# Kernel optimization log

Measured on AMD Instinct MI355X. Metric: run time of the kernel, lower is better.

## Reference

```python
import jax, jax.numpy as jnp
import numpy as np

H = 1024          # hidden_size
A = 8             # num_actions
T = 64            # timesteps
N = 256           # batch (num envs)


def _gru_cell(x, h, Wih, Whh, bih, bhh):
    # torch.nn.GRUCell math; gate order (r, z, n)
    gi = x @ Wih.T + bih           # [N, 3H]
    gh = h @ Whh.T + bhh           # [N, 3H]
    i_r, i_z, i_n = jnp.split(gi, 3, axis=1)
    h_r, h_z, h_n = jnp.split(gh, 3, axis=1)
    r = jax.nn.sigmoid(i_r + h_r)
    z = jax.nn.sigmoid(i_z + h_z)
    n = jnp.tanh(i_n + r * h_n)
    return (1.0 - z) * n + z * h


def setup_inputs() -> dict:
    key = jax.random.key(0)
    ks = jax.random.split(key, 12)
    s = 0.02
    return {
        "c": jax.random.normal(ks[0], (T * N, H), jnp.float32),
        "hxs": jax.random.normal(ks[1], (N, 3 * H), jnp.float32),
        "masks": jnp.ones((T * N, 1), jnp.float32),
        "prev_action_one_hot": jnp.zeros((T * N, A), jnp.float32).at[jnp.arange(T * N), jax.random.randint(ks[2], (T * N,), 0, A)].set(1.0),
        "h_gru_Wih": s * jax.random.normal(ks[3], (3 * H, H), jnp.float32),
        "h_gru_Whh": s * jax.random.normal(ks[4], (3 * H, H), jnp.float32),
        "h_gru_bih": jnp.zeros((3 * H,), jnp.float32),
        "h_gru_bhh": jnp.zeros((3 * H,), jnp.float32),
        "f_gru_Wih": s * jax.random.normal(ks[5], (3 * H, H), jnp.float32),
        "f_gru_Whh": s * jax.random.normal(ks[6], (3 * H, H), jnp.float32),
        "f_gru_bih": jnp.zeros((3 * H,), jnp.float32),
        "f_gru_bhh": jnp.zeros((3 * H,), jnp.float32),
        "p_W": s * jax.random.normal(ks[7], (2 * H, 2 * H + A), jnp.float32),
        "p_b": jnp.zeros((2 * H,), jnp.float32),
        "q_W": s * jax.random.normal(ks[8], (2 * H, 2 * H + A), jnp.float32),
        "q_b": jnp.zeros((2 * H,), jnp.float32),
    }


def reference(c, hxs, masks, prev_action_one_hot,
              h_gru_Wih, h_gru_Whh, h_gru_bih, h_gru_bhh,
              f_gru_Wih, f_gru_Whh, f_gru_bih, f_gru_bhh,
              p_W, p_b, q_W, q_b):
    c3 = c.reshape(T, N, H)
    m3 = masks.reshape(T, N, 1)
    a3 = prev_action_one_hot.reshape(T, N, A)
    f0 = hxs[:, :H]
    h0 = hxs[:, H:2 * H]
    q0 = hxs[:, 2 * H:]

    def step(carry, xs):
        f, h, q_mu = carry
        c_t, m_t, a_t = xs
        p_in = jnp.concatenate([h, q_mu, a_t], axis=1) * m_t
        p_dist = p_in @ p_W.T + p_b                     # [N, 2H]
        p_mu = p_dist[:, :H]
        q_in = jnp.concatenate([f, c_t, a_t], axis=1) * m_t
        q_dist = q_in @ q_W.T + q_b                     # [N, 2H]
        q_mu_new = q_dist[:, :H]
        f_new = _gru_cell(c_t, f * m_t, f_gru_Wih, f_gru_Whh, f_gru_bih, f_gru_bhh)
        h_new = _gru_cell(p_mu, h * m_t, h_gru_Wih, h_gru_Whh, h_gru_bih, h_gru_bhh)
        return (f_new, h_new, q_mu_new), (p_dist, q_dist)

    (f, h, q_mu), (p_all, q_all) = jax.lax.scan(step, (f0, h0, q0), (c3, m3, a3))
    acc_p = p_all.reshape(T * N, 2 * H)
    acc_q = q_all.reshape(T * N, 2 * H)
    hxs_out = jnp.concatenate([f, h, q_mu], axis=1)
    return acc_p, acc_q, hxs_out
```

## Files before the change

### kernel.cpp

```cpp
#include <hip/hip_runtime.h>
#include <math.h>

typedef __attribute__((ext_vector_type(8))) __bf16 bf16x8;
typedef __attribute__((ext_vector_type(4))) float f32x4;

constexpr int H = 1024, T = 64, NB = 256, TWOH = 2048, THREEH = 3072;
constexpr long long OFF_Q  = 33554432LL;
constexpr long long OFF_HX = 67108864LL;
constexpr int LA = 6;

constexpr int R_PWH = 0, R_PWQ = 2048, R_QWF = 4096, R_QWC = 6144,
              R_FWIH = 8192, R_FWHH = 11264, R_HWIH = 14336, R_HWHH = 17408;

#define LD4(p) (*reinterpret_cast<const float4*>(p))

__device__ __forceinline__ float sigf(float x) { return 1.0f / (1.0f + expf(-x)); }

__device__ __forceinline__ void gload16(const void* g, void* l) {
    __builtin_amdgcn_global_load_lds(
        (const __attribute__((address_space(1))) uint32_t*)g,
        (__attribute__((address_space(3))) uint32_t*)l, 16, 0, 0);
}

__device__ __forceinline__ void st_bf_swz(__bf16* base, int n, int k, float v) {
    base[(size_t)n * 1024 + (((k >> 3) ^ (n & 7)) << 3) + (k & 7)] = (__bf16)v;
}

#define FRAGOFF(rloc, gl) (((rloc) << 7) + ((((gl)) ^ ((rloc) & 7)) << 4))

template<int RT>
__device__ __forceinline__ void stage_tile(const char* g, char* l, int kb, int tid) {
    #pragma unroll
    for (int i = 0; i < RT / 32; ++i) {
        const int L = i * 4096 + tid * 16;
        gload16(g + (size_t)(L >> 7) * 2048 + (size_t)kb * 128 + (L & 127), l + L);
    }
}

__device__ __forceinline__ void mm128(
    int tid, char* sA, char* sB,
    const char* A, const char* B, int nit,
    f32x4 (&acc)[2][4])
{
    const int lane = tid & 63, w = tid >> 6;
    const int l15 = lane & 15, lg = lane >> 4;
    const int wr = w >> 1, wc = w & 1;
    int aoff[2][2], boff[4][2];
    #pragma unroll
    for (int fr = 0; fr < 2; ++fr)
        #pragma unroll
        for (int kk = 0; kk < 2; ++kk)
            aoff[fr][kk] = FRAGOFF(wr * 32 + fr * 16 + l15, kk * 4 + lg);
    #pragma unroll
    for (int fc = 0; fc < 4; ++fc)
        #pragma unroll
        for (int kk = 0; kk < 2; ++kk)
            boff[fc][kk] = FRAGOFF(wc * 64 + fc * 16 + l15, kk * 4 + lg);

    stage_tile<64>(A, sA, 0, tid);
    stage_tile<128>(B, sB, 0, tid);
    if (nit > 1) {
        stage_tile<64>(A, sA + 8192, 1, tid);
        stage_tile<128>(B, sB + 16384, 1, tid);
    }
    for (int kb = 0; kb < nit; ++kb) {
        const int kn = kb + 2;
        if (kn < nit) {
            const int bo = kn % 3;
            stage_tile<64>(A, sA + bo * 8192, kn, tid);
            stage_tile<128>(B, sB + bo * 16384, kn, tid);
            asm volatile("s_waitcnt vmcnt(12)" ::: "memory");
        } else if (kb + 1 < nit) {
            asm volatile("s_waitcnt vmcnt(6)" ::: "memory");
        } else {
            asm volatile("s_waitcnt vmcnt(0)" ::: "memory");
        }
        __builtin_amdgcn_s_barrier();
        __builtin_amdgcn_sched_barrier(0);
        const int bc = kb % 3;
        char* Ab = sA + bc * 8192;
        char* Bb = sB + bc * 16384;
        bf16x8 af[2][2], bv[4][2];
        #pragma unroll
        for (int fr = 0; fr < 2; ++fr)
            #pragma unroll
            for (int kk = 0; kk < 2; ++kk)
                af[fr][kk] = *reinterpret_cast<const bf16x8*>(Ab + aoff[fr][kk]);
        #pragma unroll
        for (int fc = 0; fc < 4; ++fc)
            #pragma unroll
            for (int kk = 0; kk < 2; ++kk)
                bv[fc][kk] = *reinterpret_cast<const bf16x8*>(Bb + boff[fc][kk]);
        __builtin_amdgcn_s_setprio(1);
        #pragma unroll
        for (int kk = 0; kk < 2; ++kk)
            #pragma unroll
            for (int fr = 0; fr < 2; ++fr)
                #pragma unroll
                for (int fc = 0; fc < 4; ++fc)
                    acc[fr][fc] = __builtin_amdgcn_mfma_f32_16x16x32_bf16(
                        af[fr][kk], bv[fc][kk], acc[fr][fc], 0, 0, 0);
        __builtin_amdgcn_s_setprio(0);
        __builtin_amdgcn_s_barrier();
        __builtin_amdgcn_sched_barrier(0);
    }
}

__device__ __forceinline__ void mm32g1(
    int tid, char* sA, char* sB,
    const char* A, const char* Bg,
    f32x4 (&aR)[2], f32x4 (&aZ)[2], f32x4 (&aN)[2])
{
    const int lane = tid & 63, w = tid >> 6;
    const int l15 = lane & 15, lg = lane >> 4;
    const int wr = w >> 1, wc = w & 1;
    int aoff[2], boff[2][2];
    #pragma unroll
    for (int kk = 0; kk < 2; ++kk)
        aoff[kk] = FRAGOFF(wr * 16 + l15, kk * 4 + lg);
    #pragma unroll
    for (int fc = 0; fc < 2; ++fc)
        #pragma unroll
        for (int kk = 0; kk < 2; ++kk)
            boff[fc][kk] = FRAGOFF(wc * 32 + fc * 16 + l15, kk * 4 + lg);

    auto stg = [&](int buf, int kb) {
        stage_tile<32>(A, sA + buf * 4096, kb, tid);
        #pragma unroll
        for (int g = 0; g < 3; ++g)
            stage_tile<64>(Bg + (size_t)g * 2097152, sB + buf * 24576 + g * 8192, kb, tid);
    };
    stg(0, 0);
    for (int kb = 0; kb < 16; ++kb) {
        if (kb + 1 < 16) {
            stg((kb + 1) & 1, kb + 1);
            asm volatile("s_waitcnt vmcnt(7)" ::: "memory");
        } else {
            asm volatile("s_waitcnt vmcnt(0)" ::: "memory");
        }
        __builtin_amdgcn_s_barrier();
        __builtin_amdgcn_sched_barrier(0);
        char* Ab = sA + (kb & 1) * 4096;
        char* Bb = sB + (kb & 1) * 24576;
        bf16x8 af[2];
        #pragma unroll
        for (int kk = 0; kk < 2; ++kk)
            af[kk] = *reinterpret_cast<const bf16x8*>(Ab + aoff[kk]);
        bf16x8 bvr[2][2], bvz[2][2], bvn[2][2];
        #pragma unroll
        for (int fc = 0; fc < 2; ++fc)
            #pragma unroll
            for (int kk = 0; kk < 2; ++kk) {
                bvr[fc][kk] = *reinterpret_cast<const bf16x8*>(Bb + boff[fc][kk]);
                bvz[fc][kk] = *reinterpret_cast<const bf16x8*>(Bb + 8192 + boff[fc][kk]);
                bvn[fc][kk] = *reinterpret_cast<const bf16x8*>(Bb + 16384 + boff[fc][kk]);
            }
        __builtin_amdgcn_s_setprio(1);
        #pragma unroll
        for (int kk = 0; kk < 2; ++kk)
            #pragma unroll
            for (int fc = 0; fc < 2; ++fc) {
                aR[fc] = __builtin_amdgcn_mfma_f32_16x16x32_bf16(af[kk], bvr[fc][kk], aR[fc], 0, 0, 0);
                aZ[fc] = __builtin_amdgcn_mfma_f32_16x16x32_bf16(af[kk], bvz[fc][kk], aZ[fc], 0, 0, 0);
                aN[fc] = __builtin_amdgcn_mfma_f32_16x16x32_bf16(af[kk], bvn[fc][kk], aN[fc], 0, 0, 0);
            }
        __builtin_amdgcn_s_setprio(0);
        __builtin_amdgcn_s_barrier();
        __builtin_amdgcn_sched_barrier(0);
    }
}

__device__ __forceinline__ void do_xq(int slice, int i, int tid, char* sA, char* sB,
    const char* cbfB, const char* Wb, const float* act, const float* qW, float* out)
{
    const int lane = tid & 63, w = tid >> 6;
    const int l15 = lane & 15, lg = lane >> 4;
    const int wr = w >> 1, wc = w & 1;
    const int row0 = (i >> 4) * 64, col0 = (i & 15) * 128;
    const size_t grow0 = (size_t)slice * NB + row0;
    f32x4 acc[2][4] = {};
    mm128(tid, sA, sB, cbfB + grow0 * 2048, Wb + (size_t)(R_QWC + col0) * 2048, 16, acc);
    #pragma unroll
    for (int fc = 0; fc < 4; ++fc) {
        const int gc = col0 + wc * 64 + fc * 16 + l15;
        const float* wp = qW + (size_t)gc * 2056 + 2048;
        float4 x0 = LD4(wp), x1 = LD4(wp + 4);
        #pragma unroll
        for (int fr = 0; fr < 2; ++fr)
            #pragma unroll
            for (int j = 0; j < 4; ++j) {
                const size_t n = grow0 + wr * 32 + fr * 16 + lg * 4 + j;
                const float* ar = act + n * 8;
                float4 a0 = LD4(ar), a1 = LD4(ar + 4);
                float dot = a0.x * x0.x + a0.y * x0.y + a0.z * x0.z + a0.w * x0.w
                          + a1.x * x1.x + a1.y * x1.y + a1.z * x1.z + a1.w * x1.w;
                out[OFF_Q + n * TWOH + gc] = acc[fr][fc][j] + dot;
            }
    }
}

__device__ __forceinline__ void do_gf(int slice, int i, int tid, char* sA, char* sB,
    const char* cbfB, const char* Wb, __bf16* Gfb)
{
    const int lane = tid & 63, w = tid >> 6;
    const int l15 = lane & 15, lg = lane >> 4;
    const int wr = w >> 1, wc = w & 1;
    const int row0 = (i / 24) * 64, col0 = (i % 24) * 128;
    f32x4 acc[2][4] = {};
    mm128(tid, sA, sB, cbfB + ((size_t)slice * NB + row0) * 2048,
          Wb + (size_t)(R_FWIH + col0) * 2048, 16, acc);
    __bf16* gdst = Gfb + (size_t)(slice & 7) * NB * THREEH;
    #pragma unroll
    for (int fc = 0; fc < 4; ++fc) {
        const int gc = col0 + wc * 64 + fc * 16 + l15;
        #pragma unroll
        for (int fr = 0; fr < 2; ++fr)
            #pragma unroll
            for (int j = 0; j < 4; ++j) {
                const int n = row0 + wr * 32 + fr * 16 + lg * 4 + j;
                gdst[(size_t)n * THREEH + gc] = (__bf16)acc[fr][fc][j];
            }
    }
}

__device__ __forceinline__ void do_pq(int tt, int i, int tid, char* sA, char* sB,
    const __bf16* qmu_t, const char* Wb, const float* masks, const float* act,
    const float* pW, const float* pb, float* out)
{
    const int lane = tid & 63, w = tid >> 6;
    const int l15 = lane & 15, lg = lane >> 4;
    const int wr = w >> 1, wc = w & 1;
    const int row0 = (i >> 4) * 64, col0 = (i & 15) * 128;
    f32x4 acc[2][4] = {};
    mm128(tid, sA, sB, (const char*)qmu_t + (size_t)row0 * 2048,
          Wb + (size_t)(R_PWQ + col0) * 2048, 16, acc);
    const float* mrow = masks + (size_t)tt * NB;
    float* ob = out + (size_t)tt * NB * TWOH;
    #pragma unroll
    for (int fc = 0; fc < 4; ++fc) {
        const int gc = col0 + wc * 64 + fc * 16 + l15;
        const float* wp = pW + (size_t)gc * 2056 + 2048;
        float4 x0 = LD4(wp), x1 = LD4(wp + 4);
        const float bb = pb[gc];
        #pragma unroll
        for (int fr = 0; fr < 2; ++fr)
            #pragma unroll
            for (int j = 0; j < 4; ++j) {
                const int n = row0 + wr * 32 + fr * 16 + lg * 4 + j;
                const float* ar = act + ((size_t)tt * NB + n) * 8;
                float4 a0 = LD4(ar), a1 = LD4(ar + 4);
                float dot = a0.x * x0.x + a0.y * x0.y + a0.z * x0.z + a0.w * x0.w
                          + a1.x * x1.x + a1.y * x1.y + a1.z * x1.z + a1.w * x1.w;
                ob[(size_t)n * TWOH + gc] = acc[fr][fc][j] + mrow[n] * dot + bb;
            }
    }
}

__global__ __launch_bounds__(256) void wcvt_k(
    const float* __restrict__ pW, const float* __restrict__ qW,
    const float* __restrict__ fWih, const float* __restrict__ fWhh,
    const float* __restrict__ hWih, const float* __restrict__ hWhh,
    __bf16* __restrict__ Wbf)
{
    const long i = (long)blockIdx.x * 256 + threadIdx.x;
    const int row = (int)(i >> 7);
    const int G   = (int)i & 127;
    const float* src; int stride; int koff = 0; int r;
    if (row < 2048)       { src = pW;   stride = 2056; koff = 0;    r = row; }
    else if (row < 4096)  { src = pW;   stride = 2056; koff = 1024; r = row - 2048; }
    else if (row < 6144)  { src = qW;   stride = 2056; koff = 0;    r = row - 4096; }
    else if (row < 8192)  { src = qW;   stride = 2056; koff = 1024; r = row - 6144; }
    else if (row < 11264) { src = fWih; stride = 1024; r = row - 8192; }
    else if (row < 14336) { src = fWhh; stride = 1024; r = row - 11264; }
    else if (row < 17408) { src = hWih; stride = 1024; r = row - 14336; }
    else                  { src = hWhh; stride = 1024; r = row - 17408; }
    const float* p = src + (long)r * stride + koff + G * 8;
    float4 a = LD4(p), b = LD4(p + 4);
    bf16x8 v;
    v[0] = (__bf16)a.x; v[1] = (__bf16)a.y; v[2] = (__bf16)a.z; v[3] = (__bf16)a.w;
    v[4] = (__bf16)b.x; v[5] = (__bf16)b.y; v[6] = (__bf16)b.z; v[7] = (__bf16)b.w;
    *reinterpret_cast<bf16x8*>(Wbf + (size_t)row * 1024 + ((G ^ (row & 7)) << 3)) = v;
}

__global__ __launch_bounds__(256) void ccvt_k(const float* __restrict__ c,
                                              __bf16* __restrict__ cbf) {
    const long i = (long)blockIdx.x * 256 + threadIdx.x;
    const int row = (int)(i >> 7);
    const int G   = (int)i & 127;
    const float* p = c + (size_t)row * 1024 + G * 8;
    float4 a = LD4(p), b = LD4(p + 4);
    bf16x8 v;
    v[0] = (__bf16)a.x; v[1] = (__bf16)a.y; v[2] = (__bf16)a.z; v[3] = (__bf16)a.w;
    v[4] = (__bf16)b.x; v[5] = (__bf16)b.y; v[6] = (__bf16)b.z; v[7] = (__bf16)b.w;
    *reinterpret_cast<bf16x8*>(cbf + (size_t)row * 1024 + ((G ^ (row & 7)) << 3)) = v;
}

__global__ __launch_bounds__(256) void init2_k(
    const float* __restrict__ hxs, const float* __restrict__ masks,
    float* __restrict__ fst0, float* __restrict__ hst0,
    __bf16* __restrict__ fbm0, __bf16* __restrict__ hbm0, __bf16* __restrict__ qmub0)
{
    const int idx = blockIdx.x * 256 + threadIdx.x;
    const int arr = idx >> 15;
    const int g   = idx & 32767;
    const int n   = g >> 7;
    const int G   = g & 127;
    const float m0 = masks[n];
    const float* p = hxs + (size_t)n * THREEH + arr * 1024 + G * 8;
    float4 a = LD4(p), b = LD4(p + 4);
    __bf16* dstB = arr == 0 ? fbm0 : (arr == 1 ? hbm0 : qmub0);
    bf16x8 v;
    v[0] = (__bf16)(a.x * m0); v[1] = (__bf16)(a.y * m0);
    v[2] = (__bf16)(a.z * m0); v[3] = (__bf16)(a.w * m0);
    v[4] = (__bf16)(b.x * m0); v[5] = (__bf16)(b.y * m0);
    v[6] = (__bf16)(b.z * m0); v[7] = (__bf16)(b.w * m0);
    *reinterpret_cast<bf16x8*>(dstB + (size_t)n * 1024 + ((G ^ (n & 7)) << 3)) = v;
    if (arr < 2) {
        float* dstF = arr == 0 ? fst0 : hst0;
        *reinterpret_cast<float4*>(dstF + (size_t)n * 1024 + G * 8) = a;
        *reinterpret_cast<float4*>(dstF + (size_t)n * 1024 + G * 8 + 4) = b;
    }
}

__global__ __launch_bounds__(256) void pre_k(
    const char* __restrict__ cbfB, const char* __restrict__ Wb,
    const float* __restrict__ act, const float* __restrict__ qW,
    const __bf16* __restrict__ qmb0, const float* __restrict__ masks,
    const float* __restrict__ pW, const float* __restrict__ pb,
    __bf16* __restrict__ Gfb, float* __restrict__ out)
{
    __shared__ char smem[73728];
    if (blockIdx.x < LA * 160) {
        const int s = blockIdx.x / 160;
        const int i = blockIdx.x % 160;
        if (i < 64) do_xq(s, i, threadIdx.x, smem, smem + 24576, cbfB, Wb, act, qW, out);
        else        do_gf(s, i - 64, threadIdx.x, smem, smem + 24576, cbfB, Wb, Gfb);
    } else {
        do_pq(0, blockIdx.x - LA * 160, threadIdx.x, smem, smem + 24576,
              qmb0, Wb, masks, act, pW, pb, out);
    }
}

__global__ __launch_bounds__(256) void k1_k(
    int t,
    const __bf16* __restrict__ hbm, const __bf16* __restrict__ fbm,
    __bf16* __restrict__ qmubN,
    const float* __restrict__ masks, const float* __restrict__ act,
    const float* __restrict__ qb, const float* __restrict__ qW,
    const char* __restrict__ Wb,
    __bf16* __restrict__ pmub, float* __restrict__ Shh,
    const __bf16* __restrict__ Gfb,
    const float* __restrict__ fbih, const float* __restrict__ fbhh,
    const float* __restrict__ fstF, float* __restrict__ fstN, __bf16* __restrict__ fbmN,
    float* __restrict__ out)
{
    __shared__ char smem[73728];
    char* sA = smem;
    char* sB = smem + 24576;
    const int tid = threadIdx.x;
    const int lane = tid & 63, w = tid >> 6;
    const int l15 = lane & 15, lg = lane >> 4;
    const int wr = w >> 1, wc = w & 1;
    const float* mrow = masks + (size_t)t * NB;
    const float* mn   = masks + (size_t)(t + 1 < T ? t + 1 : t) * NB;
    int b = blockIdx.x;

    if (b < 64) {
        const int row0 = (b >> 4) * 64, col0 = (b & 15) * 128;
        f32x4 acc[2][4] = {};
        mm128(tid, sA, sB,
              (const char*)hbm + (size_t)row0 * 2048,
              Wb + (size_t)(R_PWH + col0) * 2048, 16, acc);
        float* ob = out + (size_t)t * NB * TWOH;
        #pragma unroll
        for (int fc = 0; fc < 4; ++fc) {
            const int gc = col0 + wc * 64 + fc * 16 + l15;
            #pragma unroll
            for (int fr = 0; fr < 2; ++fr)
                #pragma unroll
                for (int j = 0; j < 4; ++j) {
                    const int n = row0 + wr * 32 + fr * 16 + lg * 4 + j;
                    const float v = ob[(size_t)n * TWOH + gc] + acc[fr][fc][j];
                    ob[(size_t)n * TWOH + gc] = v;
                    if (gc < 1024) st_bf_swz(pmub, n, gc, v);
                }
        }
    } else if (b < 128) {
        b -= 64;
        const int row0 = (b >> 4) * 64, col0 = (b & 15) * 128;
        f32x4 acc[2][4] = {};
        mm128(tid, sA, sB,
              (const char*)fbm + (size_t)row0 * 2048,
              Wb + (size_t)(R_QWF + col0) * 2048, 16, acc);
        float* ob = out + OFF_Q + (size_t)t * NB * TWOH;
        #pragma unroll
        for (int fc = 0; fc < 4; ++fc) {
            const int gc = col0 + wc * 64 + fc * 16 + l15;
            const float bb = qb[gc];
            #pragma unroll
            for (int fr = 0; fr < 2; ++fr)
                #pragma unroll
                for (int j = 0; j < 4; ++j) {
                    const int n = row0 + wr * 32 + fr * 16 + lg * 4 + j;
                    const float xq = ob[(size_t)n * TWOH + gc];
                    float v = acc[fr][fc][j] + mrow[n] * xq + bb;
                    ob[(size_t)n * TWOH + gc] = v;
                    if (gc < 1024) st_bf_swz(qmubN, n, gc, v * mn[n]);
                }
        }
    } else if (b < 224) {
        const int i = b - 128;
        const int row0 = (i / 24) * 64, col0 = (i % 24) * 128;
        f32x4 acc[2][4] = {};
        mm128(tid, sA, sB,
              (const char*)hbm + (size_t)row0 * 2048,
              Wb + (size_t)(R_HWHH + col0) * 2048, 16, acc);
        #pragma unroll
        for (int fc = 0; fc < 4; ++fc) {
            const int gc = col0 + wc * 64 + fc * 16 + l15;
            #pragma unroll
            for (int fr = 0; fr < 2; ++fr)
                #pragma unroll
                for (int j = 0; j < 4; ++j) {
                    const int n = row0 + wr * 32 + fr * 16 + lg * 4 + j;
                    Shh[(size_t)n * THREEH + gc] = acc[fr][fc][j];
                }
        }
    } else {
        const int i = b - 224;
        const int row0 = (i >> 4) * 32, col0 = (i & 15) * 64;
        f32x4 aR[2] = {}, aZ[2] = {}, aN[2] = {};
        mm32g1(tid, sA, sB,
               (const char*)fbm + (size_t)row0 * 2048,
               Wb + (size_t)(R_FWHH + col0) * 2048, aR, aZ, aN);
        const __bf16* gsl = Gfb + (size_t)(t & 7) * NB * THREEH;
        #pragma unroll
        for (int fc = 0; fc < 2; ++fc) {
            const int col = col0 + wc * 32 + fc * 16 + l15;
            const float br  = fbih[col] + fbhh[col];
            const float bz  = fbih[col + 1024] + fbhh[col + 1024];
            const float bni = fbih[col + 2048], bnh = fbhh[col + 2048];
            #pragma unroll
            for (int j = 0; j < 4; ++j) {
                const int n = row0 + wr * 16 + lg * 4 + j;
                const float gfr = (float)gsl[(size_t)n * THREEH + col];
                const float gfz = (float)gsl[(size_t)n * THREEH + col + 1024];
                const float gfn = (float)gsl[(size_t)n * THREEH + col + 2048];
                const float rg = sigf(gfr + aR[fc][j] + br);
                const float zg = sigf(gfz + aZ[fc][j] + bz);
                const float ng = tanhf(gfn + bni + rg * (aN[fc][j] + bnh));
                const float fm = fstF[(size_t)n * 1024 + col] * mrow[n];
                const float o = (1.f - zg) * ng + zg * fm;
                fstN[(size_t)n * 1024 + col] = o;
                st_bf_swz(fbmN, n, col, o * mn[n]);
            }
        }
    }
}

__global__ __launch_bounds__(256) void k2_k(
    int t,
    const __bf16* __restrict__ pmub, const __bf16* __restrict__ qmubN,
    const char* __restrict__ cbfB,
    const float* __restrict__ Shh,
    const float* __restrict__ hstF, float* __restrict__ hstN, __bf16* __restrict__ hbmN,
    const char* __restrict__ Wb,
    const float* __restrict__ hbih, const float* __restrict__ hbhh,
    const float* __restrict__ masks, const float* __restrict__ act,
    const float* __restrict__ pW, const float* __restrict__ pb,
    const float* __restrict__ qW,
    __bf16* __restrict__ Gfb, float* __restrict__ out)
{
    __shared__ char smem[73728];
    char* sA = smem;
    char* sB = smem + 24576;
    const int tid = threadIdx.x;
    const int lane = tid & 63, w = tid >> 6;
    const int l15 = lane & 15, lg = lane >> 4;
    const int wr = w >> 1, wc = w & 1;
    const float* mrow = masks + (size_t)t * NB;
    const float* mn   = masks + (size_t)(t + 1 < T ? t + 1 : t) * NB;
    const int b = blockIdx.x;

    if (b < 128) {
        const int row0 = (b >> 4) * 32, col0 = (b & 15) * 64;
        f32x4 aR[2] = {}, aZ[2] = {}, aN[2] = {};
        mm32g1(tid, sA, sB,
               (const char*)pmub + (size_t)row0 * 2048,
               Wb + (size_t)(R_HWIH + col0) * 2048, aR, aZ, aN);
        #pragma unroll
        for (int fc = 0; fc < 2; ++fc) {
            const int col = col0 + wc * 32 + fc * 16 + l15;
            const float bri = hbih[col],        brh = hbhh[col];
            const float bzi = hbih[col + 1024], bzh = hbhh[col + 1024];
            const float bni = hbih[col + 2048], bnh = hbhh[col + 2048];
            #pragma unroll
            for (int j = 0; j < 4; ++j) {
                const int n = row0 + wr * 16 + lg * 4 + j;
                const float ghr = Shh[(size_t)n * THREEH + col];
                const float ghz = Shh[(size_t)n * THREEH + col + 1024];
                const float ghn = Shh[(size_t)n * THREEH + col + 2048];
                const float rg = sigf(aR[fc][j] + bri + ghr + brh);
                const float zg = sigf(aZ[fc][j] + bzi + ghz + bzh);
                const float ng = tanhf(aN[fc][j] + bni + rg * (ghn + bnh));
                const float hm = hstF[(size_t)n * 1024 + col] * mrow[n];
                const float o = (1.f - zg) * ng + zg * hm;
                hstN[(size_t)n * 1024 + col] = o;
                st_bf_swz(hbmN, n, col, o * mn[n]);
            }
        }
    } else if (b < 192) {
        if (t + 1 < T)
            do_pq(t + 1, b - 128, tid, sA, sB, qmubN, Wb, masks, act, pW, pb, out);
    } else if (b < 256) {
        if (t + LA < T)
            do_xq(t + LA, b - 192, tid, sA, sB, cbfB, Wb, act, qW, out);
    } else {
        if (t + LA < T)
            do_gf(t + LA, b - 256, tid, sA, sB, cbfB, Wb, Gfb);
    }
}

__global__ __launch_bounds__(256) void write_hxs_k(const float* __restrict__ fS,
                                                   const float* __restrict__ hS,
                                                   float* out) {
    const int i = blockIdx.x * 256 + threadIdx.x;
    const int n = i / THREEH;
    const int j = i - n * THREEH;
    float v;
    if (j < H)          v = fS[(size_t)n * H + j];
    else if (j < TWOH)  v = hS[(size_t)n * H + (j - H)];
    else                v = out[OFF_Q + ((size_t)(T - 1) * NB + n) * TWOH + (j - TWOH)];
    out[OFF_HX + i] = v;
}

extern "C" void kernel_launch(void* const* d_in, const int* in_sizes, int n_in,
                              void* d_out, int out_size, void* d_ws, size_t ws_size,
                              hipStream_t stream) {
    (void)in_sizes; (void)n_in; (void)out_size; (void)ws_size;

    const float* c     = (const float*)d_in[0];
    const float* hxs   = (const float*)d_in[1];
    const float* masks = (const float*)d_in[2];
    const float* act   = (const float*)d_in[3];
    const float* hWih  = (const float*)d_in[4];
    const float* hWhh  = (const float*)d_in[5];
    const float* hbih  = (const float*)d_in[6];
    const float* hbhh  = (const float*)d_in[7];
    const float* fWih  = (const float*)d_in[8];
    const float* fWhh  = (const float*)d_in[9];
    const float* fbih  = (const float*)d_in[10];
    const float* fbhh  = (const float*)d_in[11];
    const float* pW    = (const float*)d_in[12];
    const float* pb    = (const float*)d_in[13];
    const float* qW    = (const float*)d_in[14];
    const float* qb    = (const float*)d_in[15];

    float* out = (float*)d_out;
    char*  wsb = (char*)d_ws;

    __bf16* Wbf  = (__bf16*)(wsb);
    __bf16* cbf  = (__bf16*)(wsb + 41943040LL);
    float*  fst[2] = { (float*)(wsb + 75497472LL), (float*)(wsb + 76546048LL) };
    float*  hst[2] = { (float*)(wsb + 77594624LL), (float*)(wsb + 78643200LL) };
    __bf16* fbm[2] = { (__bf16*)(wsb + 79691776LL), (__bf16*)(wsb + 80216064LL) };
    __bf16* hbm[2] = { (__bf16*)(wsb + 80740352LL), (__bf16*)(wsb + 81264640LL) };
    __bf16* qmb[2] = { (__bf16*)(wsb + 81788928LL), (__bf16*)(wsb + 82313216LL) };
    __bf16* pmub   = (__bf16*)(wsb + 82837504LL);
    float*  Shh    = (float*)(wsb + 83361792LL);
    __bf16* Gfb    = (__bf16*)(wsb + 86507520LL);
    const char* Wb   = (const char*)Wbf;
    const char* cbfB = (const char*)cbf;

    wcvt_k <<<dim3(10240), dim3(256), 0, stream>>>(pW, qW, fWih, fWhh, hWih, hWhh, Wbf);
    ccvt_k <<<dim3(8192),  dim3(256), 0, stream>>>(c, cbf);
    init2_k<<<dim3(384),   dim3(256), 0, stream>>>(hxs, masks, fst[0], hst[0],
                                                   fbm[0], hbm[0], qmb[0]);
    pre_k  <<<dim3(LA * 160 + 64), dim3(256), 0, stream>>>(
        cbfB, Wb, act, qW, qmb[0], masks, pW, pb, Gfb, out);

    for (int t = 0; t < T; ++t) {
        const int cur = t & 1, nxt = cur ^ 1;
        k1_k<<<dim3(352), dim3(256), 0, stream>>>(
            t, hbm[cur], fbm[cur], qmb[nxt],
            masks, act, qb, qW, Wb, pmub, Shh, Gfb,
            fbih, fbhh, fst[cur], fst[nxt], fbm[nxt], out);
        k2_k<<<dim3(352), dim3(256), 0, stream>>>(
            t, pmub, qmb[nxt], cbfB, Shh,
            hst[cur], hst[nxt], hbm[nxt],
            Wb, hbih, hbhh, masks, act, pW, pb, qW, Gfb, out);
    }

    write_hxs_k<<<dim3(3072), dim3(256), 0, stream>>>(fst[0], hst[0], out);
}
```

Measured before the change: 2.107 ms.

## Enlarge GEMM tiles to 128x128 and 64-row GRU tiles with triple-buffered LDS

Adds an mm128r2 routine that computes 128x128 output tiles with a three-stage LDS pipeline. It uses this for the Whh and Wih-gate GEMMs. The fused GRU gate GEMM grows from 32 to 64 rows per block (mm64g3), also triple-buffered. Both changes reduce the block count per step kernel from 352 to 240 and raise data reuse per staged tile. In exchange, LDS per block rises to 96KB and register pressure goes up, which lowers occupancy and leaves fewer blocks to fill the 256 CUs.

```diff
diff --git a/kernel.cpp b/kernel.cpp
--- a/kernel.cpp
+++ b/kernel.cpp
@@ -106,46 +106,111 @@
     }
 }
 
-__device__ __forceinline__ void mm32g1(
+__device__ __forceinline__ void mm128r2(
+    int tid, char* sA, char* sB,
+    const char* A, const char* B,
+    f32x4 (&acc)[4][4])
+{
+    const int lane = tid & 63, w = tid >> 6;
+    const int l15 = lane & 15, lg = lane >> 4;
+    const int wr = w >> 1, wc = w & 1;
+    int aoff[4][2], boff[4][2];
+    #pragma unroll
+    for (int f = 0; f < 4; ++f)
+        #pragma unroll
+        for (int kk = 0; kk < 2; ++kk) {
+            aoff[f][kk] = FRAGOFF(wr * 64 + f * 16 + l15, kk * 4 + lg);
+            boff[f][kk] = FRAGOFF(wc * 64 + f * 16 + l15, kk * 4 + lg);
+        }
+    stage_tile<128>(A, sA, 0, tid);
+    stage_tile<128>(B, sB, 0, tid);
+    stage_tile<128>(A, sA + 16384, 1, tid);
+    stage_tile<128>(B, sB + 16384, 1, tid);
+    for (int kb = 0; kb < 16; ++kb) {
+        const int kn = kb + 2;
+        if (kn < 16) {
+            const int bo = kn % 3;
+            stage_tile<128>(A, sA + bo * 16384, kn, tid);
+            stage_tile<128>(B, sB + bo * 16384, kn, tid);
+            asm volatile("s_waitcnt vmcnt(16)" ::: "memory");
+        } else if (kb + 1 < 16) {
+            asm volatile("s_waitcnt vmcnt(8)" ::: "memory");
+        } else {
+            asm volatile("s_waitcnt vmcnt(0)" ::: "memory");
+        }
+        __builtin_amdgcn_s_barrier();
+        __builtin_amdgcn_sched_barrier(0);
+        const int bc = kb % 3;
+        char* Ab = sA + bc * 16384;
+        char* Bb = sB + bc * 16384;
+        bf16x8 af[4][2], bv[4][2];
+        #pragma unroll
+        for (int f = 0; f < 4; ++f)
+            #pragma unroll
+            for (int kk = 0; kk < 2; ++kk) {
+                af[f][kk] = *reinterpret_cast<const bf16x8*>(Ab + aoff[f][kk]);
+                bv[f][kk] = *reinterpret_cast<const bf16x8*>(Bb + boff[f][kk]);
+            }
+        __builtin_amdgcn_s_setprio(1);
+        #pragma unroll
+        for (int kk = 0; kk < 2; ++kk)
+            #pragma unroll
+            for (int fr = 0; fr < 4; ++fr)
+                #pragma unroll
+                for (int fc = 0; fc < 4; ++fc)
+                    acc[fr][fc] = __builtin_amdgcn_mfma_f32_16x16x32_bf16(
+                        af[fr][kk], bv[fc][kk], acc[fr][fc], 0, 0, 0);
+        __builtin_amdgcn_s_setprio(0);
+        __builtin_amdgcn_s_barrier();
+        __builtin_amdgcn_sched_barrier(0);
+    }
+}
+
+__device__ __forceinline__ void mm64g3(
     int tid, char* sA, char* sB,
     const char* A, const char* Bg,
-    f32x4 (&aR)[2], f32x4 (&aZ)[2], f32x4 (&aN)[2])
-{
-    const int lane = tid & 63, w = tid >> 6;
-    const int l15 = lane & 15, lg = lane >> 4;
-    const int wr = w >> 1, wc = w & 1;
-    int aoff[2], boff[2][2];
-    #pragma unroll
-    for (int kk = 0; kk < 2; ++kk)
-        aoff[kk] = FRAGOFF(wr * 16 + l15, kk * 4 + lg);
-    #pragma unroll
-    for (int fc = 0; fc < 2; ++fc)
-        #pragma unroll
-        for (int kk = 0; kk < 2; ++kk)
-            boff[fc][kk] = FRAGOFF(wc * 32 + fc * 16 + l15, kk * 4 + lg);
-
+    f32x4 (&aR)[2][2], f32x4 (&aZ)[2][2], f32x4 (&aN)[2][2])
+{
+    const int lane = tid & 63, w = tid >> 6;
+    const int l15 = lane & 15, lg = lane >> 4;
+    const int wr = w >> 1, wc = w & 1;
+    int aoff[2][2], boff[2][2];
+    #pragma unroll
+    for (int f = 0; f < 2; ++f)
+        #pragma unroll
+        for (int kk = 0; kk < 2; ++kk) {
+            aoff[f][kk] = FRAGOFF(wr * 32 + f * 16 + l15, kk * 4 + lg);
+            boff[f][kk] = FRAGOFF(wc * 32 + f * 16 + l15, kk * 4 + lg);
+        }
     auto stg = [&](int buf, int kb) {
-        stage_tile<32>(A, sA + buf * 4096, kb, tid);
+        stage_tile<64>(A, sA + buf * 8192, kb, tid);
         #pragma unroll
         for (int g = 0; g < 3; ++g)
             stage_tile<64>(Bg + (size_t)g * 2097152, sB + buf * 24576 + g * 8192, kb, tid);
     };
     stg(0, 0);
+    stg(1, 1);
     for (int kb = 0; kb < 16; ++kb) {
-        if (kb + 1 < 16) {
-            stg((kb + 1) & 1, kb + 1);
-            asm volatile("s_waitcnt vmcnt(7)" ::: "memory");
+        const int kn = kb + 2;
+        if (kn < 16) {
+            stg(kn % 3, kn);
+            asm volatile("s_waitcnt vmcnt(16)" ::: "memory");
+        } else if (kb + 1 < 16) {
+            asm volatile("s_waitcnt vmcnt(8)" ::: "memory");
         } else {
             asm volatile("s_waitcnt vmcnt(0)" ::: "memory");
         }
         __builtin_amdgcn_s_barrier();
         __builtin_amdgcn_sched_barrier(0);
-        char* Ab = sA + (kb & 1) * 4096;
-        char* Bb = sB + (kb & 1) * 24576;
-        bf16x8 af[2];
-        #pragma unroll
-        for (int kk = 0; kk < 2; ++kk)
-            af[kk] = *reinterpret_cast<const bf16x8*>(Ab + aoff[kk]);
+        const int bc = kb % 3;
+        char* Ab = sA + bc * 8192;
+        char* Bb = sB + bc * 24576;
+        bf16x8 af[2][2];
+        #pragma unroll
+        for (int f = 0; f < 2; ++f)
+            #pragma unroll
+            for (int kk = 0; kk < 2; ++kk)
+                af[f][kk] = *reinterpret_cast<const bf16x8*>(Ab + aoff[f][kk]);
         bf16x8 bvr[2][2], bvz[2][2], bvn[2][2];
         #pragma unroll
         for (int fc = 0; fc < 2; ++fc)
@@ -159,11 +224,13 @@
         #pragma unroll
         for (int kk = 0; kk < 2; ++kk)
             #pragma unroll
-            for (int fc = 0; fc < 2; ++fc) {
-                aR[fc] = __builtin_amdgcn_mfma_f32_16x16x32_bf16(af[kk], bvr[fc][kk], aR[fc], 0, 0, 0);
-                aZ[fc] = __builtin_amdgcn_mfma_f32_16x16x32_bf16(af[kk], bvz[fc][kk], aZ[fc], 0, 0, 0);
-                aN[fc] = __builtin_amdgcn_mfma_f32_16x16x32_bf16(af[kk], bvn[fc][kk], aN[fc], 0, 0, 0);
-            }
+            for (int fr = 0; fr < 2; ++fr)
+                #pragma unroll
+                for (int fc = 0; fc < 2; ++fc) {
+                    aR[fr][fc] = __builtin_amdgcn_mfma_f32_16x16x32_bf16(af[fr][kk], bvr[fc][kk], aR[fr][fc], 0, 0, 0);
+                    aZ[fr][fc] = __builtin_amdgcn_mfma_f32_16x16x32_bf16(af[fr][kk], bvz[fc][kk], aZ[fr][fc], 0, 0, 0);
+                    aN[fr][fc] = __builtin_amdgcn_mfma_f32_16x16x32_bf16(af[fr][kk], bvn[fc][kk], aN[fr][fc], 0, 0, 0);
+                }
         __builtin_amdgcn_s_setprio(0);
         __builtin_amdgcn_s_barrier();
         __builtin_amdgcn_sched_barrier(0);
@@ -205,19 +272,19 @@
     const int lane = tid & 63, w = tid >> 6;
     const int l15 = lane & 15, lg = lane >> 4;
     const int wr = w >> 1, wc = w & 1;
-    const int row0 = (i / 24) * 64, col0 = (i % 24) * 128;
-    f32x4 acc[2][4] = {};
-    mm128(tid, sA, sB, cbfB + ((size_t)slice * NB + row0) * 2048,
-          Wb + (size_t)(R_FWIH + col0) * 2048, 16, acc);
+    const int row0 = (i / 24) * 128, col0 = (i % 24) * 128;
+    f32x4 acc[4][4] = {};
+    mm128r2(tid, sA, sB, cbfB + ((size_t)slice * NB + row0) * 2048,
+            Wb + (size_t)(R_FWIH + col0) * 2048, acc);
     __bf16* gdst = Gfb + (size_t)(slice & 7) * NB * THREEH;
     #pragma unroll
     for (int fc = 0; fc < 4; ++fc) {
         const int gc = col0 + wc * 64 + fc * 16 + l15;
         #pragma unroll
-        for (int fr = 0; fr < 2; ++fr)
+        for (int fr = 0; fr < 4; ++fr)
             #pragma unroll
             for (int j = 0; j < 4; ++j) {
-                const int n = row0 + wr * 32 + fr * 16 + lg * 4 + j;
+                const int n = row0 + wr * 64 + fr * 16 + lg * 4 + j;
                 gdst[(size_t)n * THREEH + gc] = (__bf16)acc[fr][fc][j];
             }
     }
@@ -329,14 +396,15 @@
     const float* __restrict__ pW, const float* __restrict__ pb,
     __bf16* __restrict__ Gfb, float* __restrict__ out)
 {
-    __shared__ char smem[73728];
-    if (blockIdx.x < LA * 160) {
-        const int s = blockIdx.x / 160;
-        const int i = blockIdx.x % 160;
+    __shared__ char smem[98304];
+    const int b = blockIdx.x;
+    if (b < LA * 112) {
+        const int s = b / 112;
+        const int i = b % 112;
         if (i < 64) do_xq(s, i, threadIdx.x, smem, smem + 24576, cbfB, Wb, act, qW, out);
-        else        do_gf(s, i - 64, threadIdx.x, smem, smem + 24576, cbfB, Wb, Gfb);
+        else        do_gf(s, i - 64, threadIdx.x, smem, smem + 49152, cbfB, Wb, Gfb);
     } else {
-        do_pq(0, blockIdx.x - LA * 160, threadIdx.x, smem, smem + 24576,
+        do_pq(0, b - LA * 112, threadIdx.x, smem, smem + 24576,
               qmb0, Wb, masks, act, pW, pb, out);
     }
 }
@@ -354,9 +422,7 @@
     const float* __restrict__ fstF, float* __restrict__ fstN, __bf16* __restrict__ fbmN,
     float* __restrict__ out)
 {
-    __shared__ char smem[73728];
-    char* sA = smem;
-    char* sB = smem + 24576;
+    __shared__ char smem[98304];
     const int tid = threadIdx.x;
     const int lane = tid & 63, w = tid >> 6;
     const int l15 = lane & 15, lg = lane >> 4;
@@ -368,7 +434,7 @@
     if (b < 64) {
         const int row0 = (b >> 4) * 64, col0 = (b & 15) * 128;
         f32x4 acc[2][4] = {};
-        mm128(tid, sA, sB,
+        mm128(tid, smem, smem + 24576,
               (const char*)hbm + (size_t)row0 * 2048,
               Wb + (size_t)(R_PWH + col0) * 2048, 16, acc);
         float* ob = out + (size_t)t * NB * TWOH;
@@ -389,7 +455,7 @@
         b -= 64;
         const int row0 = (b >> 4) * 64, col0 = (b & 15) * 128;
         f32x4 acc[2][4] = {};
-        mm128(tid, sA, sB,
+        mm128(tid, smem, smem + 24576,
               (const char*)fbm + (size_t)row0 * 2048,
               Wb + (size_t)(R_QWF + col0) * 2048, 16, acc);
         float* ob = out + OFF_Q + (size_t)t * NB * TWOH;
@@ -408,29 +474,29 @@
                     if (gc < 1024) st_bf_swz(qmubN, n, gc, v * mn[n]);
                 }
         }
-    } else if (b < 224) {
+    } else if (b < 176) {
         const int i = b - 128;
-        const int row0 = (i / 24) * 64, col0 = (i % 24) * 128;
-        f32x4 acc[2][4] = {};
-        mm128(tid, sA, sB,
-              (const char*)hbm + (size_t)row0 * 2048,
-              Wb + (size_t)(R_HWHH + col0) * 2048, 16, acc);
+        const int row0 = (i / 24) * 128, col0 = (i % 24) * 128;
+        f32x4 acc[4][4] = {};
+        mm128r2(tid, smem, smem + 49152,
+                (const char*)hbm + (size_t)row0 * 2048,
+                Wb + (size_t)(R_HWHH + col0) * 2048, acc);
         #pragma unroll
         for (int fc = 0; fc < 4; ++fc) {
             const int gc = col0 + wc * 64 + fc * 16 + l15;
             #pragma unroll
-            for (int fr = 0; fr < 2; ++fr)
+            for (int fr = 0; fr < 4; ++fr)
                 #pragma unroll
                 for (int j = 0; j < 4; ++j) {
-                    const int n = row0 + wr * 32 + fr * 16 + lg * 4 + j;
+                    const int n = row0 + wr * 64 + fr * 16 + lg * 4 + j;
                     Shh[(size_t)n * THREEH + gc] = acc[fr][fc][j];
                 }
         }
     } else {
-        const int i = b - 224;
-        const int row0 = (i >> 4) * 32, col0 = (i & 15) * 64;
-        f32x4 aR[2] = {}, aZ[2] = {}, aN[2] = {};
-        mm32g1(tid, sA, sB,
+        const int i = b - 176;
+        const int row0 = (i >> 4) * 64, col0 = (i & 15) * 64;
+        f32x4 aR[2][2] = {}, aZ[2][2] = {}, aN[2][2] = {};
+        mm64g3(tid, smem, smem + 24576,
                (const char*)fbm + (size_t)row0 * 2048,
                Wb + (size_t)(R_FWHH + col0) * 2048, aR, aZ, aN);
         const __bf16* gsl = Gfb + (size_t)(t & 7) * NB * THREEH;
@@ -441,19 +507,21 @@
             const float bz  = fbih[col + 1024] + fbhh[col + 1024];
             const float bni = fbih[col + 2048], bnh = fbhh[col + 2048];
             #pragma unroll
-            for (int j = 0; j < 4; ++j) {
-                const int n = row0 + wr * 16 + lg * 4 + j;
-                const float gfr = (float)gsl[(size_t)n * THREEH + col];
-                const float gfz = (float)gsl[(size_t)n * THREEH + col + 1024];
-                const float gfn = (float)gsl[(size_t)n * THREEH + col + 2048];
-                const float rg = sigf(gfr + aR[fc][j] + br);
-                const float zg = sigf(gfz + aZ[fc][j] + bz);
-                const float ng = tanhf(gfn + bni + rg * (aN[fc][j] + bnh));
-                const float fm = fstF[(size_t)n * 1024 + col] * mrow[n];
-                const float o = (1.f - zg) * ng + zg * fm;
-                fstN[(size_t)n * 1024 + col] = o;
-                st_bf_swz(fbmN, n, col, o * mn[n]);
-            }
+            for (int fr = 0; fr < 2; ++fr)
+                #pragma unroll
+                for (int j = 0; j < 4; ++j) {
+                    const int n = row0 + wr * 32 + fr * 16 + lg * 4 + j;
+                    const float gfr = (float)gsl[(size_t)n * THREEH + col];
+                    const float gfz = (float)gsl[(size_t)n * THREEH + col + 1024];
+                    const float gfn = (float)gsl[(size_t)n * THREEH + col + 2048];
+                    const float rg = sigf(gfr + aR[fr][fc][j] + br);
+                    const float zg = sigf(gfz + aZ[fr][fc][j] + bz);
+                    const float ng = tanhf(gfn + bni + rg * (aN[fr][fc][j] + bnh));
+                    const float fm = fstF[(size_t)n * 1024 + col] * mrow[n];
+                    const float o = (1.f - zg) * ng + zg * fm;
+                    fstN[(size_t)n * 1024 + col] = o;
+                    st_bf_swz(fbmN, n, col, o * mn[n]);
+                }
         }
     }
 }
@@ -471,9 +539,7 @@
     const float* __restrict__ qW,
     __bf16* __restrict__ Gfb, float* __restrict__ out)
 {
-    __shared__ char smem[73728];
-    char* sA = smem;
-    char* sB = smem + 24576;
+    __shared__ char smem[98304];
     const int tid = threadIdx.x;
     const int lane = tid & 63, w = tid >> 6;
     const int l15 = lane & 15, lg = lane >> 4;
@@ -482,10 +548,10 @@
     const float* mn   = masks + (size_t)(t + 1 < T ? t + 1 : t) * NB;
     const int b = blockIdx.x;
 
-    if (b < 128) {
-        const int row0 = (b >> 4) * 32, col0 = (b & 15) * 64;
-        f32x4 aR[2] = {}, aZ[2] = {}, aN[2] = {};
-        mm32g1(tid, sA, sB,
+    if (b < 64) {
+        const int row0 = (b >> 4) * 64, col0 = (b & 15) * 64;
+        f32x4 aR[2][2] = {}, aZ[2][2] = {}, aN[2][2] = {};
+        mm64g3(tid, smem, smem + 24576,
                (const char*)pmub + (size_t)row0 * 2048,
                Wb + (size_t)(R_HWIH + col0) * 2048, aR, aZ, aN);
         #pragma unroll
@@ -495,29 +561,31 @@
             const float bzi = hbih[col + 1024], bzh = hbhh[col + 1024];
             const float bni = hbih[col + 2048], bnh = hbhh[col + 2048];
             #pragma unroll
-            for (int j = 0; j < 4; ++j) {
-                const int n = row0 + wr * 16 + lg * 4 + j;
-                const float ghr = Shh[(size_t)n * THREEH + col];
-                const float ghz = Shh[(size_t)n * THREEH + col + 1024];
-                const float ghn = Shh[(size_t)n * THREEH + col + 2048];
-                const float rg = sigf(aR[fc][j] + bri + ghr + brh);
-                const float zg = sigf(aZ[fc][j] + bzi + ghz + bzh);
-                const float ng = tanhf(aN[fc][j] + bni + rg * (ghn + bnh));
-                const float hm = hstF[(size_t)n * 1024 + col] * mrow[n];
-                const float o = (1.f - zg) * ng + zg * hm;
-                hstN[(size_t)n * 1024 + col] = o;
-                st_bf_swz(hbmN, n, col, o * mn[n]);
-            }
-        }
+            for (int fr = 0; fr < 2; ++fr)
+                #pragma unroll
+                for (int j = 0; j < 4; ++j) {
+                    const int n = row0 + wr * 32 + fr * 16 + lg * 4 + j;
+                    const float ghr = Shh[(size_t)n * THREEH + col];
+                    const float ghz = Shh[(size_t)n * THREEH + col + 1024];
+                    const float ghn = Shh[(size_t)n * THREEH + col + 2048];
+                    const float rg = sigf(aR[fr][fc][j] + bri + ghr + brh);
+                    const float zg = sigf(aZ[fr][fc][j] + bzi + ghz + bzh);
+                    const float ng = tanhf(aN[fr][fc][j] + bni + rg * (ghn + bnh));
+                    const float hm = hstF[(size_t)n * 1024 + col] * mrow[n];
+                    const float o = (1.f - zg) * ng + zg * hm;
+                    hstN[(size_t)n * 1024 + col] = o;
+                    st_bf_swz(hbmN, n, col, o * mn[n]);
+                }
+        }
+    } else if (b < 128) {
+        if (t + 1 < T)
+            do_pq(t + 1, b - 64, tid, smem, smem + 24576, qmubN, Wb, masks, act, pW, pb, out);
     } else if (b < 192) {
-        if (t + 1 < T)
-            do_pq(t + 1, b - 128, tid, sA, sB, qmubN, Wb, masks, act, pW, pb, out);
-    } else if (b < 256) {
         if (t + LA < T)
-            do_xq(t + LA, b - 192, tid, sA, sB, cbfB, Wb, act, qW, out);
+            do_xq(t + LA, b - 128, tid, smem, smem + 24576, cbfB, Wb, act, qW, out);
     } else {
         if (t + LA < T)
-            do_gf(t + LA, b - 256, tid, sA, sB, cbfB, Wb, Gfb);
+            do_gf(t + LA, b - 192, tid, smem, smem + 49152, cbfB, Wb, Gfb);
     }
 }
 
@@ -576,16 +644,16 @@
     ccvt_k <<<dim3(8192),  dim3(256), 0, stream>>>(c, cbf);
     init2_k<<<dim3(384),   dim3(256), 0, stream>>>(hxs, masks, fst[0], hst[0],
                                                    fbm[0], hbm[0], qmb[0]);
-    pre_k  <<<dim3(LA * 160 + 64), dim3(256), 0, stream>>>(
+    pre_k  <<<dim3(LA * 112 + 64), dim3(256), 0, stream>>>(
         cbfB, Wb, act, qW, qmb[0], masks, pW, pb, Gfb, out);
 
     for (int t = 0; t < T; ++t) {
         const int cur = t & 1, nxt = cur ^ 1;
-        k1_k<<<dim3(352), dim3(256), 0, stream>>>(
+        k1_k<<<dim3(240), dim3(256), 0, stream>>>(
             t, hbm[cur], fbm[cur], qmb[nxt],
             masks, act, qb, qW, Wb, pmub, Shh, Gfb,
             fbih, fbhh, fst[cur], fst[nxt], fbm[nxt], out);
-        k2_k<<<dim3(352), dim3(256), 0, stream>>>(
+        k2_k<<<dim3(240), dim3(256), 0, stream>>>(
             t, pmub, qmb[nxt], cbfB, Shh,
             hst[cur], hst[nxt], hbm[nxt],
             Wb, hbih, hbhh, masks, act, pW, pb, qW, Gfb, out);
```

Result: slower. 2.434 ms (+15.5%).
